# Performance work log

Measured on AMD Instinct MI355X. Metric: run time of the kernel, lower is better.

The kernel has to match this reference:

```python
import jax, jax.numpy as jnp
import numpy as np

B, L, E, D, A = 256, 196, 2048, 1024, 512


def setup_inputs() -> dict:
    key = jax.random.key(0)
    ks = jax.random.split(key, 9)
    enc_scale = 1.0 / np.sqrt(E)
    dec_scale = 1.0 / np.sqrt(D)
    att_scale = 1.0 / np.sqrt(A)
    return {
        "encoder_out": jax.random.normal(ks[0], (B, L, E), dtype=jnp.float32),
        "decoder_hidden": jax.random.normal(ks[1], (B, D), dtype=jnp.float32),
        "mask1": jax.random.randint(ks[2], (B, L), 0, 2, dtype=jnp.int32),
        "We": jax.random.uniform(ks[3], (E, A), jnp.float32, -enc_scale, enc_scale),
        "be": jax.random.uniform(ks[4], (A,), jnp.float32, -enc_scale, enc_scale),
        "Wd": jax.random.uniform(ks[5], (D, A), jnp.float32, -dec_scale, dec_scale),
        "bd": jax.random.uniform(ks[6], (A,), jnp.float32, -dec_scale, dec_scale),
        "wf": jax.random.uniform(ks[7], (A,), jnp.float32, -att_scale, att_scale),
        "bf": jax.random.uniform(ks[8], (), jnp.float32, -att_scale, att_scale),
    }


def reference(encoder_out, decoder_hidden, mask1, We, be, Wd, bd, wf, bf):
    # att1: [B, L, A]; att2: [B, A]
    att1 = jnp.einsum('ble,ea->bla', encoder_out, We) + be
    att2 = jnp.einsum('bd,da->ba', decoder_hidden, Wd) + bd
    # scores: [B, L]
    att = jnp.einsum('bla,a->bl', jnp.tanh(att1 + att2[:, None, :]), wf) + bf
    att = jnp.where(mask1 == 0, jnp.float32(-1e9), att)
    alpha = jax.nn.softmax(att, axis=1)
    # weighted sum over regions: [B, E]
    awe = jnp.einsum('ble,bl->be', encoder_out, alpha)
    return (awe, alpha)
```

## Files before the change

kernel.cpp:

```cpp
#include <hip/hip_runtime.h>
#include <hip/hip_bf16.h>


#define B_ 256
#define L_ 196
#define E_ 2048
#define D_ 1024
#define A_ 512
#define M_TOT (B_ * L_)

typedef __attribute__((ext_vector_type(8))) short bf16x8;
typedef __attribute__((ext_vector_type(4))) float f32x4;

static __device__ __forceinline__ unsigned short f2bf(float f) {
    union { float f; unsigned u; } u{f};
    unsigned r = u.u + 0x7fffu + ((u.u >> 16) & 1u);
    return (unsigned short)(r >> 16);
}

static __device__ __forceinline__ void gload_lds16(const void* g, void* l) {
    __builtin_amdgcn_global_load_lds(
        (const __attribute__((address_space(1))) unsigned int*)g,
        (__attribute__((address_space(3))) unsigned int*)l, 16, 0, 0);
}

__global__ __launch_bounds__(256) void k_wepack(const float* __restrict__ We,
                                                unsigned short* __restrict__ WeP) {
    int i = blockIdx.x * 256 + threadIdx.x;
    int k = i >> 9, n = i & 511;
    int kb = k >> 5, kg = (k >> 3) & 3, e = k & 7;
    int kgE = kg ^ ((n >> 1) & 3);
    WeP[(kb << 14) + (n << 5) + (kgE << 3) + e] = f2bf(We[i]);
}

__global__ __launch_bounds__(256) void k_bias2(const float* __restrict__ dec,
                                               const float* __restrict__ Wd,
                                               const float* __restrict__ be,
                                               const float* __restrict__ bd,
                                               float* __restrict__ bias2) {
    int b = blockIdx.x, t = threadIdx.x;
    __shared__ float ds[D_];
    for (int i = t; i < D_; i += 256) ds[i] = dec[b * D_ + i];
    __syncthreads();
    for (int a0 = 0; a0 < A_; a0 += 256) {
        int a = a0 + t;
        float acc = 0.f;
        #pragma unroll 8
        for (int d = 0; d < D_; d++) acc += ds[d] * Wd[d * A_ + a];
        bias2[b * A_ + a] = acc + be[a] + bd[a];
    }
}

__global__ __launch_bounds__(512, 4) void k_gemm_score(
        const float* __restrict__ enc,
        const unsigned short* __restrict__ WeP,
        const float* __restrict__ bias2,
        const float* __restrict__ wf,
        float* __restrict__ scores) {
    __shared__ __align__(16) unsigned short aL[2][64 * 32];
    __shared__ __align__(16) unsigned short bL[2][512 * 32];
    __shared__ float score_lds[64];

    const int tid = threadIdx.x;
    const int m0 = blockIdx.x * 64;
    const int lane = tid & 63;
    const int wid = tid >> 6;
    const int kg = lane >> 4, lr = lane & 15;

    const int ar = tid >> 3, ak = (tid & 7) << 2;
    const float* aSrc = enc + (size_t)(m0 + ar) * E_ + ak;
    const int aoff = ar * 32 + (ak ^ (((ar >> 1) & 3) << 3));

    const unsigned short* bSrcLane = WeP + (size_t)(wid * 512 + lane * 8);

    auto stageB = [&](int kb, int buf) {
        const unsigned short* s = bSrcLane + ((size_t)kb << 14);
        unsigned short* d = &bL[buf][wid * 512];
        #pragma unroll
        for (int i = 0; i < 4; i++)
            gload_lds16(s + i * 4096, d + i * 4096);
    };
    auto writeA = [&](const float4& v, int buf) {
        short4 p;
        p.x = (short)f2bf(v.x); p.y = (short)f2bf(v.y);
        p.z = (short)f2bf(v.z); p.w = (short)f2bf(v.w);
        *reinterpret_cast<short4*>(&aL[buf][aoff]) = p;
    };

    f32x4 acc[4][4];
    #pragma unroll
    for (int i = 0; i < 4; i++)
        #pragma unroll
        for (int j = 0; j < 4; j++) acc[i][j] = (f32x4){0.f, 0.f, 0.f, 0.f};

    auto computeTile = [&](int buf) {
        bf16x8 bfr[4];
        #pragma unroll
        for (int j = 0; j < 4; j++) {
            int n = wid * 64 + j * 16 + lr;
            bfr[j] = *reinterpret_cast<const bf16x8*>(
                &bL[buf][n * 32 + ((kg ^ ((n >> 1) & 3)) << 3)]);
        }
        #pragma unroll
        for (int i = 0; i < 4; i++) {
            int row = i * 16 + lr;
            bf16x8 af = *reinterpret_cast<const bf16x8*>(
                &aL[buf][row * 32 + ((kg ^ ((row >> 1) & 3)) << 3)]);
            #pragma unroll
            for (int j = 0; j < 4; j++)
                acc[i][j] = __builtin_amdgcn_mfma_f32_16x16x32_bf16(
                    af, bfr[j], acc[i][j], 0, 0, 0);
        }
    };

    stageB(0, 0);
    __builtin_amdgcn_sched_barrier(0);
    float4 av0  = *reinterpret_cast<const float4*>(aSrc);
    float4 avH1 = *reinterpret_cast<const float4*>(aSrc + 32);
    float4 avH2 = *reinterpret_cast<const float4*>(aSrc + 64);
    writeA(av0, 0);
    asm volatile("s_waitcnt vmcnt(2) lgkmcnt(0)" ::: "memory");
    __builtin_amdgcn_s_barrier();
    __builtin_amdgcn_sched_barrier(0);

    int buf = 0;
    for (int t = 0; t < 63; t++) {
        stageB(t + 1, buf ^ 1);
        __builtin_amdgcn_sched_barrier(0);
        int tn = (t + 3 > 63) ? 63 : t + 3;
        float4 avN = *reinterpret_cast<const float4*>(aSrc + tn * 32);
        __builtin_amdgcn_sched_barrier(0);
        computeTile(buf);
        writeA(avH1, buf ^ 1);
        asm volatile("s_waitcnt vmcnt(1) lgkmcnt(0)" ::: "memory");
        __builtin_amdgcn_s_barrier();
        __builtin_amdgcn_sched_barrier(0);
        avH1 = avH2; avH2 = avN;
        buf ^= 1;
    }
    computeTile(buf);

    if (tid < 64) score_lds[tid] = 0.f;
    __syncthreads();
    #pragma unroll
    for (int i = 0; i < 4; i++) {
        #pragma unroll
        for (int r = 0; r < 4; r++) {
            int R = i * 16 + kg * 4 + r;
            int gm = m0 + R;
            int bg = gm / L_;
            float sum = 0.f;
            #pragma unroll
            for (int j = 0; j < 4; j++) {
                int C = wid * 64 + j * 16 + lr;
                float x = acc[i][j][r] + bias2[bg * A_ + C];
                float ex = __expf(2.f * x);
                float th = 1.f - 2.f * __builtin_amdgcn_rcpf(ex + 1.f);
                sum += wf[C] * th;
            }
            #pragma unroll
            for (int mk = 1; mk < 16; mk <<= 1) sum += __shfl_xor(sum, mk);
            if (lr == 0) atomicAdd(&score_lds[R], sum);
        }
    }
    __syncthreads();
    if (tid < 64) scores[m0 + tid] = score_lds[tid];
}

__global__ __launch_bounds__(256) void k_softmax(const float* __restrict__ scores,
                                                 const int* __restrict__ mask,
                                                 const float* __restrict__ bfp,
                                                 float* __restrict__ alpha) {
    int b = blockIdx.x, t = threadIdx.x;
    float bfv = bfp[0];
    float v = -INFINITY;
    if (t < L_) v = (mask[b * L_ + t] == 0) ? -1e9f : (scores[b * L_ + t] + bfv);
    __shared__ float redm[4], reds[4];
    float m = v;
    #pragma unroll
    for (int s = 1; s < 64; s <<= 1) m = fmaxf(m, __shfl_xor(m, s));
    int w = t >> 6;
    if ((t & 63) == 0) redm[w] = m;
    __syncthreads();
    m = fmaxf(fmaxf(redm[0], redm[1]), fmaxf(redm[2], redm[3]));
    float e = (t < L_) ? expf(v - m) : 0.f;
    float s = e;
    #pragma unroll
    for (int k = 1; k < 64; k <<= 1) s += __shfl_xor(s, k);
    if ((t & 63) == 0) reds[w] = s;
    __syncthreads();
    s = reds[0] + reds[1] + reds[2] + reds[3];
    if (t < L_) alpha[b * L_ + t] = e / s;
}

__global__ __launch_bounds__(256) void k_awe(const float* __restrict__ enc,
                                             const float* __restrict__ alpha,
                                             float* __restrict__ awe) {
    int b = blockIdx.y, ec = blockIdx.x, t = threadIdx.x;
    int g = t >> 6, lt = t & 63;
    __shared__ float al[L_];
    __shared__ float4 red[256];
    if (t < L_) al[t] = alpha[b * L_ + t];
    __syncthreads();
    int e0 = (ec << 8) + (lt << 2);
    const float* base = enc + (size_t)b * L_ * E_ + e0;
    float4 acc = {0.f, 0.f, 0.f, 0.f};
    int l0 = g * 49;
    #pragma unroll 7
    for (int l = l0; l < l0 + 49; l++) {
        float4 v = *reinterpret_cast<const float4*>(base + (size_t)l * E_);
        float a = al[l];
        acc.x += a * v.x; acc.y += a * v.y; acc.z += a * v.z; acc.w += a * v.w;
    }
    red[t] = acc;
    __syncthreads();
    if (t < 64) {
        float4 r0 = red[t], r1 = red[64 + t], r2 = red[128 + t], r3 = red[192 + t];
        float4 o;
        o.x = r0.x + r1.x + r2.x + r3.x;
        o.y = r0.y + r1.y + r2.y + r3.y;
        o.z = r0.z + r1.z + r2.z + r3.z;
        o.w = r0.w + r1.w + r2.w + r3.w;
        *reinterpret_cast<float4*>(awe + b * E_ + (ec << 8) + (t << 2)) = o;
    }
}

extern "C" void kernel_launch(void* const* d_in, const int* in_sizes, int n_in,
                              void* d_out, int out_size, void* d_ws, size_t ws_size,
                              hipStream_t stream) {
    const float* enc  = (const float*)d_in[0];
    const float* dec  = (const float*)d_in[1];
    const int*   mask = (const int*)d_in[2];
    const float* We   = (const float*)d_in[3];
    const float* be   = (const float*)d_in[4];
    const float* Wd   = (const float*)d_in[5];
    const float* bd   = (const float*)d_in[6];
    const float* wf   = (const float*)d_in[7];
    const float* bf   = (const float*)d_in[8];

    float* awe   = (float*)d_out;
    float* alpha = awe + (size_t)B_ * E_;

    char* ws = (char*)d_ws;
    unsigned short* WeP = (unsigned short*)ws;
    float* bias2  = (float*)(ws + (2u << 20));
    float* scores = (float*)(ws + (2u << 20) + (512u << 10));

    hipLaunchKernelGGL(k_wepack, dim3((E_ * A_) / 256), dim3(256), 0, stream, We, WeP);
    hipLaunchKernelGGL(k_bias2, dim3(B_), dim3(256), 0, stream, dec, Wd, be, bd, bias2);
    hipLaunchKernelGGL(k_gemm_score, dim3(M_TOT / 64), dim3(512), 0, stream,
                       enc, WeP, bias2, wf, scores);
    hipLaunchKernelGGL(k_softmax, dim3(B_), dim3(256), 0, stream, scores, mask, bf, alpha);
    hipLaunchKernelGGL(k_awe, dim3(8, B_), dim3(256), 0, stream, enc, alpha, awe);
}
```

Measured before the change: 395.6 us.

## Retile score GEMM to 128x128 tiles with N-split partial scores

The score GEMM is restructured from 64-row blocks covering all 512 columns to 128x128 tiles with four column tiles per row block. Each tile writes a partial score, and the softmax kernel sums the four partials. Block indices are swizzled so the column tiles of a row block run close together and share the encoder rows in L2. The A-load now uses packed bf16 conversion, and the awe kernel switches to one 512-thread block per batch with 4-way unrolled accumulators. The trade is re-reading each encoder row once per column tile, plus extra partial-score traffic, in exchange for better per-block operand reuse and more parallel blocks.

```diff
diff --git a/kernel.cpp b/kernel.cpp
--- a/kernel.cpp
+++ b/kernel.cpp
@@ -16,6 +16,11 @@
     union { float f; unsigned u; } u{f};
     unsigned r = u.u + 0x7fffu + ((u.u >> 16) & 1u);
     return (unsigned short)(r >> 16);
+}
+
+static __device__ __forceinline__ unsigned int pk2(float x, float y) {
+    __hip_bfloat162 h = __float22bfloat162_rn(float2{x, y});
+    return *reinterpret_cast<unsigned int*>(&h);
 }
 
 static __device__ __forceinline__ void gload_lds16(const void* g, void* l) {
@@ -51,40 +56,57 @@
     }
 }
 
-__global__ __launch_bounds__(512, 4) void k_gemm_score(
+__global__ __launch_bounds__(256, 3) void k_gemm_score(
         const float* __restrict__ enc,
         const unsigned short* __restrict__ WeP,
         const float* __restrict__ bias2,
         const float* __restrict__ wf,
-        float* __restrict__ scores) {
-    __shared__ __align__(16) unsigned short aL[2][64 * 32];
-    __shared__ __align__(16) unsigned short bL[2][512 * 32];
-    __shared__ float score_lds[64];
+        float* __restrict__ scoresP) {
+    __shared__ __align__(16) unsigned short aL[2][128 * 32];
+    __shared__ __align__(16) unsigned short bL[2][128 * 32];
+    __shared__ float score_lds[4][64];
 
     const int tid = threadIdx.x;
-    const int m0 = blockIdx.x * 64;
+    const int raw = blockIdx.x;
+    const int wg = (raw & 7) * 196 + (raw >> 3);
+    const int mt = wg >> 2, nt = wg & 3;
+    const int m0 = mt * 128;
+
     const int lane = tid & 63;
     const int wid = tid >> 6;
+    const int wm = wid >> 1, wn = wid & 1;
     const int kg = lane >> 4, lr = lane & 15;
 
-    const int ar = tid >> 3, ak = (tid & 7) << 2;
-    const float* aSrc = enc + (size_t)(m0 + ar) * E_ + ak;
-    const int aoff = ar * 32 + (ak ^ (((ar >> 1) & 3) << 3));
-
-    const unsigned short* bSrcLane = WeP + (size_t)(wid * 512 + lane * 8);
+    const int ar = tid >> 1, kh = tid & 1;
+    const float* aSrc = enc + (size_t)(m0 + ar) * E_ + kh * 16;
+    const int sw = (ar >> 1) & 3;
+    const int aOff0 = ar * 32 + (((kh * 2 + 0) ^ sw) << 3);
+    const int aOff1 = ar * 32 + (((kh * 2 + 1) ^ sw) << 3);
+
+    const unsigned short* bSrcLane =
+        WeP + nt * 4096 + (size_t)(wid * 1024 + lane * 8);
 
     auto stageB = [&](int kb, int buf) {
         const unsigned short* s = bSrcLane + ((size_t)kb << 14);
-        unsigned short* d = &bL[buf][wid * 512];
-        #pragma unroll
-        for (int i = 0; i < 4; i++)
-            gload_lds16(s + i * 4096, d + i * 4096);
-    };
-    auto writeA = [&](const float4& v, int buf) {
-        short4 p;
-        p.x = (short)f2bf(v.x); p.y = (short)f2bf(v.y);
-        p.z = (short)f2bf(v.z); p.w = (short)f2bf(v.w);
-        *reinterpret_cast<short4*>(&aL[buf][aoff]) = p;
+        #pragma unroll
+        for (int c = 0; c < 2; c++)
+            gload_lds16(s + c * 512, &bL[buf][(wid * 2 + c) * 512]);
+    };
+    auto loadA = [&](float4 (&v)[4], int t) {
+        const float* p = aSrc + t * 32;
+        v[0] = *reinterpret_cast<const float4*>(p);
+        v[1] = *reinterpret_cast<const float4*>(p + 4);
+        v[2] = *reinterpret_cast<const float4*>(p + 8);
+        v[3] = *reinterpret_cast<const float4*>(p + 12);
+    };
+    auto writeA = [&](const float4 (&v)[4], int buf) {
+        uint4 lo, hi;
+        lo.x = pk2(v[0].x, v[0].y); lo.y = pk2(v[0].z, v[0].w);
+        lo.z = pk2(v[1].x, v[1].y); lo.w = pk2(v[1].z, v[1].w);
+        hi.x = pk2(v[2].x, v[2].y); hi.y = pk2(v[2].z, v[2].w);
+        hi.z = pk2(v[3].x, v[3].y); hi.w = pk2(v[3].z, v[3].w);
+        *reinterpret_cast<uint4*>(&aL[buf][aOff0]) = lo;
+        *reinterpret_cast<uint4*>(&aL[buf][aOff1]) = hi;
     };
 
     f32x4 acc[4][4];
@@ -97,13 +119,13 @@
         bf16x8 bfr[4];
         #pragma unroll
         for (int j = 0; j < 4; j++) {
-            int n = wid * 64 + j * 16 + lr;
+            int n = wn * 64 + j * 16 + lr;
             bfr[j] = *reinterpret_cast<const bf16x8*>(
                 &bL[buf][n * 32 + ((kg ^ ((n >> 1) & 3)) << 3)]);
         }
         #pragma unroll
         for (int i = 0; i < 4; i++) {
-            int row = i * 16 + lr;
+            int row = wm * 64 + i * 16 + lr;
             bf16x8 af = *reinterpret_cast<const bf16x8*>(
                 &aL[buf][row * 32 + ((kg ^ ((row >> 1) & 3)) << 3)]);
             #pragma unroll
@@ -115,11 +137,12 @@
 
     stageB(0, 0);
     __builtin_amdgcn_sched_barrier(0);
-    float4 av0  = *reinterpret_cast<const float4*>(aSrc);
-    float4 avH1 = *reinterpret_cast<const float4*>(aSrc + 32);
-    float4 avH2 = *reinterpret_cast<const float4*>(aSrc + 64);
+    float4 av0[4], avH1[4], avH2[4];
+    loadA(av0, 0);
+    loadA(avH1, 1);
+    loadA(avH2, 2);
     writeA(av0, 0);
-    asm volatile("s_waitcnt vmcnt(2) lgkmcnt(0)" ::: "memory");
+    asm volatile("s_waitcnt vmcnt(8) lgkmcnt(0)" ::: "memory");
     __builtin_amdgcn_s_barrier();
     __builtin_amdgcn_sched_barrier(0);
 
@@ -128,53 +151,61 @@
         stageB(t + 1, buf ^ 1);
         __builtin_amdgcn_sched_barrier(0);
         int tn = (t + 3 > 63) ? 63 : t + 3;
-        float4 avN = *reinterpret_cast<const float4*>(aSrc + tn * 32);
+        float4 avN[4];
+        loadA(avN, tn);
         __builtin_amdgcn_sched_barrier(0);
         computeTile(buf);
         writeA(avH1, buf ^ 1);
-        asm volatile("s_waitcnt vmcnt(1) lgkmcnt(0)" ::: "memory");
+        asm volatile("s_waitcnt vmcnt(4) lgkmcnt(0)" ::: "memory");
         __builtin_amdgcn_s_barrier();
         __builtin_amdgcn_sched_barrier(0);
-        avH1 = avH2; avH2 = avN;
+        #pragma unroll
+        for (int q = 0; q < 4; q++) { avH1[q] = avH2[q]; avH2[q] = avN[q]; }
         buf ^= 1;
     }
     computeTile(buf);
 
-    if (tid < 64) score_lds[tid] = 0.f;
-    __syncthreads();
     #pragma unroll
     for (int i = 0; i < 4; i++) {
         #pragma unroll
         for (int r = 0; r < 4; r++) {
-            int R = i * 16 + kg * 4 + r;
-            int gm = m0 + R;
+            int Rw = i * 16 + kg * 4 + r;
+            int gm = m0 + wm * 64 + Rw;
             int bg = gm / L_;
             float sum = 0.f;
             #pragma unroll
             for (int j = 0; j < 4; j++) {
-                int C = wid * 64 + j * 16 + lr;
+                int C = nt * 128 + wn * 64 + j * 16 + lr;
                 float x = acc[i][j][r] + bias2[bg * A_ + C];
                 float ex = __expf(2.f * x);
-                float th = 1.f - 2.f * __builtin_amdgcn_rcpf(ex + 1.f);
-                sum += wf[C] * th;
+                sum += wf[C] * (1.f - 2.f * __builtin_amdgcn_rcpf(ex + 1.f));
             }
             #pragma unroll
             for (int mk = 1; mk < 16; mk <<= 1) sum += __shfl_xor(sum, mk);
-            if (lr == 0) atomicAdd(&score_lds[R], sum);
+            if (lr == 0) score_lds[wid][Rw] = sum;
         }
     }
     __syncthreads();
-    if (tid < 64) scores[m0 + tid] = score_lds[tid];
-}
-
-__global__ __launch_bounds__(256) void k_softmax(const float* __restrict__ scores,
+    if (tid < 128) {
+        int wmp = tid >> 6;
+        float s = score_lds[wmp * 2][tid & 63] + score_lds[wmp * 2 + 1][tid & 63];
+        scoresP[nt * M_TOT + m0 + tid] = s;
+    }
+}
+
+__global__ __launch_bounds__(256) void k_softmax(const float* __restrict__ scoresP,
                                                  const int* __restrict__ mask,
                                                  const float* __restrict__ bfp,
                                                  float* __restrict__ alpha) {
     int b = blockIdx.x, t = threadIdx.x;
     float bfv = bfp[0];
     float v = -INFINITY;
-    if (t < L_) v = (mask[b * L_ + t] == 0) ? -1e9f : (scores[b * L_ + t] + bfv);
+    if (t < L_) {
+        int idx = b * L_ + t;
+        float sc = scoresP[idx] + scoresP[M_TOT + idx] +
+                   scoresP[2 * M_TOT + idx] + scoresP[3 * M_TOT + idx];
+        v = (mask[idx] == 0) ? -1e9f : (sc + bfv);
+    }
     __shared__ float redm[4], reds[4];
     float m = v;
     #pragma unroll
@@ -193,36 +224,32 @@
     if (t < L_) alpha[b * L_ + t] = e / s;
 }
 
-__global__ __launch_bounds__(256) void k_awe(const float* __restrict__ enc,
+__global__ __launch_bounds__(512) void k_awe(const float* __restrict__ enc,
                                              const float* __restrict__ alpha,
                                              float* __restrict__ awe) {
-    int b = blockIdx.y, ec = blockIdx.x, t = threadIdx.x;
-    int g = t >> 6, lt = t & 63;
+    int b = blockIdx.x, t = threadIdx.x;
     __shared__ float al[L_];
-    __shared__ float4 red[256];
     if (t < L_) al[t] = alpha[b * L_ + t];
     __syncthreads();
-    int e0 = (ec << 8) + (lt << 2);
-    const float* base = enc + (size_t)b * L_ * E_ + e0;
-    float4 acc = {0.f, 0.f, 0.f, 0.f};
-    int l0 = g * 49;
-    #pragma unroll 7
-    for (int l = l0; l < l0 + 49; l++) {
-        float4 v = *reinterpret_cast<const float4*>(base + (size_t)l * E_);
-        float a = al[l];
-        acc.x += a * v.x; acc.y += a * v.y; acc.z += a * v.z; acc.w += a * v.w;
-    }
-    red[t] = acc;
-    __syncthreads();
-    if (t < 64) {
-        float4 r0 = red[t], r1 = red[64 + t], r2 = red[128 + t], r3 = red[192 + t];
-        float4 o;
-        o.x = r0.x + r1.x + r2.x + r3.x;
-        o.y = r0.y + r1.y + r2.y + r3.y;
-        o.z = r0.z + r1.z + r2.z + r3.z;
-        o.w = r0.w + r1.w + r2.w + r3.w;
-        *reinterpret_cast<float4*>(awe + b * E_ + (ec << 8) + (t << 2)) = o;
-    }
+    const float* base = enc + (size_t)b * L_ * E_ + t * 4;
+    float4 a0 = {0.f, 0.f, 0.f, 0.f}, a1 = a0, a2 = a0, a3 = a0;
+    for (int l = 0; l < L_; l += 4) {
+        float4 v0 = *reinterpret_cast<const float4*>(base + (size_t)l * E_);
+        float4 v1 = *reinterpret_cast<const float4*>(base + (size_t)(l + 1) * E_);
+        float4 v2 = *reinterpret_cast<const float4*>(base + (size_t)(l + 2) * E_);
+        float4 v3 = *reinterpret_cast<const float4*>(base + (size_t)(l + 3) * E_);
+        float c0 = al[l], c1 = al[l + 1], c2 = al[l + 2], c3 = al[l + 3];
+        a0.x += c0 * v0.x; a0.y += c0 * v0.y; a0.z += c0 * v0.z; a0.w += c0 * v0.w;
+        a1.x += c1 * v1.x; a1.y += c1 * v1.y; a1.z += c1 * v1.z; a1.w += c1 * v1.w;
+        a2.x += c2 * v2.x; a2.y += c2 * v2.y; a2.z += c2 * v2.z; a2.w += c2 * v2.w;
+        a3.x += c3 * v3.x; a3.y += c3 * v3.y; a3.z += c3 * v3.z; a3.w += c3 * v3.w;
+    }
+    float4 o;
+    o.x = (a0.x + a1.x) + (a2.x + a3.x);
+    o.y = (a0.y + a1.y) + (a2.y + a3.y);
+    o.z = (a0.z + a1.z) + (a2.z + a3.z);
+    o.w = (a0.w + a1.w) + (a2.w + a3.w);
+    *reinterpret_cast<float4*>(awe + (size_t)b * E_ + t * 4) = o;
 }
 
 extern "C" void kernel_launch(void* const* d_in, const int* in_sizes, int n_in,
@@ -243,13 +270,13 @@
 
     char* ws = (char*)d_ws;
     unsigned short* WeP = (unsigned short*)ws;
-    float* bias2  = (float*)(ws + (2u << 20));
-    float* scores = (float*)(ws + (2u << 20) + (512u << 10));
+    float* bias2   = (float*)(ws + (2u << 20));
+    float* scoresP = (float*)(ws + (2u << 20) + (512u << 10));
 
     hipLaunchKernelGGL(k_wepack, dim3((E_ * A_) / 256), dim3(256), 0, stream, We, WeP);
     hipLaunchKernelGGL(k_bias2, dim3(B_), dim3(256), 0, stream, dec, Wd, be, bd, bias2);
-    hipLaunchKernelGGL(k_gemm_score, dim3(M_TOT / 64), dim3(512), 0, stream,
-                       enc, WeP, bias2, wf, scores);
-    hipLaunchKernelGGL(k_softmax, dim3(B_), dim3(256), 0, stream, scores, mask, bf, alpha);
-    hipLaunchKernelGGL(k_awe, dim3(8, B_), dim3(256), 0, stream, enc, alpha, awe);
-}
+    hipLaunchKernelGGL(k_gemm_score, dim3((M_TOT / 128) * 4), dim3(256), 0, stream,
+                       enc, WeP, bias2, wf, scoresP);
+    hipLaunchKernelGGL(k_softmax, dim3(B_), dim3(256), 0, stream, scoresP, mask, bf, alpha);
+    hipLaunchKernelGGL(k_awe, dim3(B_), dim3(512), 0, stream, enc, alpha, awe);
+}
```

Result: slower. 450.1 us (+13.8%).
